# Optimization experiments

Hardware: AMD Instinct MI355X
Metric: run time of the kernel (lower is better)

The kernel has to match this reference:

```python
import jax, jax.numpy as jnp
import numpy as np

SIGMA = 5.0


def setup_inputs() -> dict:
    key = jax.random.key(0)
    ks = jax.random.split(key, 10)
    D, H, K0, K1 = 2048, 2048, 16, 8
    return {
        "inputs": jax.random.normal(ks[0], (1, D), jnp.float32),
        "cluster_center": jax.random.normal(ks[1], (K0, D), jnp.float32),
        "leaf_weight_u": jax.random.normal(ks[2], (K0, D, H), jnp.float32),
        "leaf_bias_u": jax.random.normal(ks[3], (K0, H), jnp.float32),
        "no_leaf_weight_i": jax.random.normal(ks[4], (K1, H), jnp.float32),
        "no_leaf_bias_i": jax.random.normal(ks[5], (K1,), jnp.float32),
        "no_leaf_weight_u": jax.random.normal(ks[6], (K1, H, H), jnp.float32),
        "no_leaf_bias_u": jax.random.normal(ks[7], (K1, H), jnp.float32),
        "root_weight_u": jax.random.normal(ks[8], (H, H), jnp.float32),
        "root_bias_u": jax.random.normal(ks[9], (1, H), jnp.float32),
    }


def reference(inputs, cluster_center, leaf_weight_u, leaf_bias_u,
              no_leaf_weight_i, no_leaf_bias_i, no_leaf_weight_u,
              no_leaf_bias_u, root_weight_u, root_bias_u):
    x = inputs[0]  # (D,)
    # soft assignment to cluster centers: exp(-||x-c||^2/(2*sigma)) / sum(...)
    diff = x[None, :] - cluster_center               # (K0, D)
    sq = jnp.sum(diff * diff, axis=-1)               # (K0,)
    assign = jax.nn.softmax(-sq / (2.0 * SIGMA))     # (K0,)
    # leaf cells: assignment-weighted tanh projections
    value_u = jnp.tanh(jnp.einsum('d,kdh->kh', x, leaf_weight_u) + leaf_bias_u)  # (K0, H)
    c_leaf = assign[:, None] * value_u               # (K0, H)
    # non-leaf gating: softmax over cluster_layer_1 per leaf
    gate_logits = jnp.einsum('kh,jh->kj', c_leaf, no_leaf_weight_i) + no_leaf_bias_i[None, :]  # (K0, K1)
    gate = jax.nn.softmax(gate_logits, axis=1)       # (K0, K1)
    u = jnp.tanh(jnp.einsum('kh,jhg->kjg', c_leaf, no_leaf_weight_u) + no_leaf_bias_u[None, :, :])  # (K0, K1, H)
    c_no_leaf = jnp.sum(gate[:, :, None] * u, axis=0)  # sum over K0 -> (K1, H)
    # root: sum over cluster_layer_1
    root = jnp.tanh(c_no_leaf @ root_weight_u + root_bias_u)  # (K1, H)
    root_c = jnp.sum(root, axis=0, keepdims=True)    # (1, H)
    return (root_c, root_c)
```

## Files before the change

### kernel.cpp

```cpp
#include <hip/hip_runtime.h>
#include <math.h>

#define D   2048
#define H   2048
#define K0  16
#define KJ  8

#define SKIP_THR 1e-7f

#define WS_ASSIGN 0
#define WS_GATE   64
#define WS_CLEAF  256
#define WS_PLEAF  33024
#define WS_PNL    1081600
#define WS_CNL    5275904
#define WS_PROOT  5292288
#define WS_TMP    5816576

__global__ void k_assign(const float* __restrict__ x, const float* __restrict__ cc,
                         float* __restrict__ ws) {
    int t = threadIdx.x, w = t >> 6, l = t & 63;
    const float4* c4 = (const float4*)(cc + w * D);
    const float4* x4 = (const float4*)x;
    float a = 0.f;
#pragma unroll
    for (int i = 0; i < 8; ++i) {
        float4 xv = x4[l + i * 64];
        float4 cv = c4[l + i * 64];
        float dx = xv.x - cv.x, dy = xv.y - cv.y;
        float dz = xv.z - cv.z, dw = xv.w - cv.w;
        a += dx * dx + dy * dy + dz * dz + dw * dw;
    }
#pragma unroll
    for (int off = 32; off > 0; off >>= 1) a += __shfl_down(a, off);
    __shared__ float sq[K0];
    if (l == 0) sq[w] = a;
    __syncthreads();
    if (t == 0) {
        float v[K0], m = -1e30f;
#pragma unroll
        for (int k = 0; k < K0; ++k) { v[k] = -sq[k] * 0.1f; m = fmaxf(m, v[k]); }
        float s = 0.f;
#pragma unroll
        for (int k = 0; k < K0; ++k) { v[k] = expf(v[k] - m); s += v[k]; }
        float inv = 1.0f / s;
#pragma unroll
        for (int k = 0; k < K0; ++k) ws[WS_ASSIGN + k] = v[k] * inv;
    }
}

__global__ void k_leaf_partial(const float* __restrict__ x, const float* __restrict__ W,
                               float* __restrict__ ws) {
    const int k = blockIdx.x;
    if (ws[WS_ASSIGN + k] < SKIP_THR) return;
    const int h0 = blockIdx.y * 1024;
    const int d0 = blockIdx.z * 64;
    __shared__ float xs[64];
    int t = threadIdx.x;
    if (t < 64) xs[t] = x[d0 + t];
    __syncthreads();
    int h = h0 + t * 4;
    const float* Wp = W + ((size_t)k * D + d0) * (size_t)H + h;
    float4 acc = make_float4(0.f, 0.f, 0.f, 0.f);
#pragma unroll 16
    for (int dd = 0; dd < 64; ++dd) {
        float4 w = *(const float4*)(Wp + (size_t)dd * H);
        float xv = xs[dd];
        acc.x += xv * w.x; acc.y += xv * w.y; acc.z += xv * w.z; acc.w += xv * w.w;
    }
    *(float4*)(ws + WS_PLEAF + ((size_t)(blockIdx.z * K0 + k) << 11) + h) = acc;
}

__global__ void k_cleaf(const float* __restrict__ lb, float* __restrict__ ws) {
    int idx = blockIdx.x * 256 + threadIdx.x;
    int k = idx >> 11, h = idx & (H - 1);
    float az = ws[WS_ASSIGN + k];
    float v = 0.f;
    if (az >= SKIP_THR) {
        float s = 0.f;
#pragma unroll
        for (int dc = 0; dc < 32; ++dc)
            s += ws[WS_PLEAF + ((size_t)(dc * K0 + k) << 11) + h];
        v = tanhf(s + lb[k * H + h]) * az;
    }
    ws[WS_CLEAF + k * H + h] = v;
}

__global__ void k_gate(const float* __restrict__ Wi, const float* __restrict__ bi,
                       float* __restrict__ ws) {
    int k = blockIdx.x;
    int t = threadIdx.x;
    const float* cl = ws + WS_CLEAF + k * H;
    float acc[KJ];
#pragma unroll
    for (int j = 0; j < KJ; ++j) acc[j] = 0.f;
    for (int h = t; h < H; h += 256) {
        float c = cl[h];
#pragma unroll
        for (int j = 0; j < KJ; ++j) acc[j] += c * Wi[j * H + h];
    }
    __shared__ float red[KJ][256];
#pragma unroll
    for (int j = 0; j < KJ; ++j) red[j][t] = acc[j];
    __syncthreads();
    for (int s = 128; s > 0; s >>= 1) {
        if (t < s) {
#pragma unroll
            for (int j = 0; j < KJ; ++j) red[j][t] += red[j][t + s];
        }
        __syncthreads();
    }
    if (t == 0) {
        float l[KJ], m = -1e30f;
#pragma unroll
        for (int j = 0; j < KJ; ++j) { l[j] = red[j][0] + bi[j]; m = fmaxf(m, l[j]); }
        float s = 0.f;
#pragma unroll
        for (int j = 0; j < KJ; ++j) { l[j] = expf(l[j] - m); s += l[j]; }
        float inv = 1.0f / s;
#pragma unroll
        for (int j = 0; j < KJ; ++j) ws[WS_GATE + k * KJ + j] = l[j] * inv;
    }
}

__global__ void k_nl_partial(const float* __restrict__ Wn, float* __restrict__ ws) {
    const int j  = blockIdx.x;
    const int g0 = blockIdx.y * 512;
    const int h0 = blockIdx.z * 128;
    __shared__ float cls[K0][128];
    int t = threadIdx.x;
    for (int i = t; i < K0 * 128; i += 256) {
        int k = i >> 7, hh = i & 127;
        cls[k][hh] = ws[WS_CLEAF + k * H + h0 + hh];
    }
    __syncthreads();
    int g = g0 + t * 2;
    const float* Wp = Wn + ((size_t)j * H + h0) * (size_t)H + g;
    float2 acc[K0];
#pragma unroll
    for (int k = 0; k < K0; ++k) { acc[k].x = 0.f; acc[k].y = 0.f; }
#pragma unroll 8
    for (int hh = 0; hh < 128; ++hh) {
        float2 w = *(const float2*)(Wp + (size_t)hh * H);
#pragma unroll
        for (int k = 0; k < K0; ++k) {
            float c = cls[k][hh];
            acc[k].x += c * w.x; acc[k].y += c * w.y;
        }
    }
#pragma unroll
    for (int k = 0; k < K0; ++k)
        *(float2*)(ws + WS_PNL + ((size_t)((blockIdx.z * KJ + j) * K0 + k) << 11) + g) = acc[k];
}

__global__ void k_cnl(const float* __restrict__ nb, float* __restrict__ ws) {
    int idx = blockIdx.x * 128 + threadIdx.x;
    int j = idx >> 11, g = idx & (H - 1);
    float bias = nb[j * H + g];
    float out = 0.f;
#pragma unroll
    for (int k = 0; k < K0; ++k) {
        float s = 0.f;
#pragma unroll
        for (int hc = 0; hc < 16; ++hc)
            s += ws[WS_PNL + ((size_t)((hc * KJ + j) * K0 + k) << 11) + g];
        out += ws[WS_GATE + k * KJ + j] * tanhf(s + bias);
    }
    ws[WS_CNL + j * H + g] = out;
}

__global__ void k_root_partial(const float* __restrict__ Wr, float* __restrict__ ws) {
    const int g2t = blockIdx.x;
    const int g0  = blockIdx.y * 64;
    __shared__ float cns[KJ][64];
    int t = threadIdx.x;
    for (int i = t; i < KJ * 64; i += 256) {
        int j = i >> 6, gg = i & 63;
        cns[j][gg] = ws[WS_CNL + j * H + g0 + gg];
    }
    __syncthreads();
    int g2 = g2t * 512 + t * 2;
    float2 acc[KJ];
#pragma unroll
    for (int j = 0; j < KJ; ++j) { acc[j].x = 0.f; acc[j].y = 0.f; }
#pragma unroll 8
    for (int gg = 0; gg < 64; ++gg) {
        float2 w = *(const float2*)(Wr + (size_t)(g0 + gg) * H + g2);
#pragma unroll
        for (int j = 0; j < KJ; ++j) {
            float c = cns[j][gg];
            acc[j].x += c * w.x; acc[j].y += c * w.y;
        }
    }
#pragma unroll
    for (int j = 0; j < KJ; ++j)
        *(float2*)(ws + WS_PROOT + ((size_t)(blockIdx.y * KJ + j) << 11) + g2) = acc[j];
}

__global__ void k_root_tanh(const float* __restrict__ rb, float* __restrict__ ws) {
    int j  = blockIdx.x;
    int g2 = blockIdx.y * 256 + threadIdx.x;
    float s = 0.f;
#pragma unroll
    for (int gc = 0; gc < 32; ++gc)
        s += ws[WS_PROOT + ((size_t)(gc * KJ + j) << 11) + g2];
    ws[WS_TMP + j * H + g2] = tanhf(s + rb[g2]);
}

__global__ void k_final(float* __restrict__ ws, float* __restrict__ out) {
    int g2 = blockIdx.x * 256 + threadIdx.x;
    float tot = 0.f;
#pragma unroll
    for (int j = 0; j < KJ; ++j) tot += ws[WS_TMP + j * H + g2];
    out[g2] = tot;
    out[H + g2] = tot;
}

extern "C" void kernel_launch(void* const* d_in, const int* in_sizes, int n_in,
                              void* d_out, int out_size, void* d_ws, size_t ws_size,
                              hipStream_t stream) {
    const float* x  = (const float*)d_in[0];
    const float* cc = (const float*)d_in[1];
    const float* lw = (const float*)d_in[2];
    const float* lb = (const float*)d_in[3];
    const float* wi = (const float*)d_in[4];
    const float* bi = (const float*)d_in[5];
    const float* wn = (const float*)d_in[6];
    const float* nb = (const float*)d_in[7];
    const float* wr = (const float*)d_in[8];
    const float* rb = (const float*)d_in[9];
    float* out = (float*)d_out;
    float* ws  = (float*)d_ws;

    k_assign      <<<1, 1024, 0, stream>>>(x, cc, ws);
    k_leaf_partial<<<dim3(16, 2, 32), 256, 0, stream>>>(x, lw, ws);
    k_cleaf       <<<128, 256, 0, stream>>>(lb, ws);
    k_gate        <<<16, 256, 0, stream>>>(wi, bi, ws);
    k_nl_partial  <<<dim3(8, 4, 16), 256, 0, stream>>>(wn, ws);
    k_cnl         <<<128, 128, 0, stream>>>(nb, ws);
    k_root_partial<<<dim3(4, 32), 256, 0, stream>>>(wr, ws);
    k_root_tanh   <<<dim3(8, 8), 256, 0, stream>>>(rb, ws);
    k_final       <<<8, 256, 0, stream>>>(ws, out);
}
```

Measured before the change: 500.9 us.

## Fuse all stages into one cooperative kernel with grid-wide syncs

Replaces the nine separate kernel launches with a single cooperative kernel of 512 blocks. The stages are separated by grid.sync, and the assignment softmax is recomputed in every block from the stored squared distances. The goal is to remove per-launch overhead and inter-kernel gaps. The cost is grid-sync latency, fixed work partitioning that leaves many blocks idle in the small stages, and a launch-bounds occupancy constraint. The original multi-kernel path stays as a fallback if the cooperative launch fails.

```diff
diff --git a/kernel.cpp b/kernel.cpp
--- a/kernel.cpp
+++ b/kernel.cpp
@@ -1,5 +1,8 @@
 #include <hip/hip_runtime.h>
+#include <hip/hip_cooperative_groups.h>
 #include <math.h>
+
+namespace cg = cooperative_groups;
 
 #define D   2048
 #define H   2048
@@ -8,7 +11,9 @@
 
 #define SKIP_THR 1e-7f
 
-#define WS_ASSIGN 0
+#define NBLK 512
+
+#define WS_SQ     0
 #define WS_GATE   64
 #define WS_CLEAF  256
 #define WS_PLEAF  33024
@@ -17,6 +22,212 @@
 #define WS_PROOT  5292288
 #define WS_TMP    5816576
 
+__device__ __forceinline__ void calc_assign(const float* __restrict__ ws, float a[K0]) {
+    float m = -1e30f;
+#pragma unroll
+    for (int k = 0; k < K0; ++k) { a[k] = -ws[WS_SQ + k] * 0.1f; m = fmaxf(m, a[k]); }
+    float s = 0.f;
+#pragma unroll
+    for (int k = 0; k < K0; ++k) { a[k] = expf(a[k] - m); s += a[k]; }
+    float inv = 1.0f / s;
+#pragma unroll
+    for (int k = 0; k < K0; ++k) a[k] *= inv;
+}
+
+__global__ __launch_bounds__(256, 2) void fused_kernel(
+    const float* __restrict__ x,  const float* __restrict__ cc,
+    const float* __restrict__ lw, const float* __restrict__ lb,
+    const float* __restrict__ wi, const float* __restrict__ bi,
+    const float* __restrict__ wn, const float* __restrict__ nb,
+    const float* __restrict__ wr, const float* __restrict__ rb,
+    float* __restrict__ out, float* __restrict__ ws)
+{
+    cg::grid_group grid = cg::this_grid();
+    __shared__ float smem[2048];
+    const int bid = blockIdx.x, t = threadIdx.x;
+
+    if (bid < K0) {
+        const float4* x4 = (const float4*)x;
+        const float4* c4 = (const float4*)(cc + bid * D);
+        float acc = 0.f;
+#pragma unroll
+        for (int i = 0; i < 2; ++i) {
+            float4 xv = x4[t + 256 * i], cv = c4[t + 256 * i];
+            float dx = xv.x - cv.x, dy = xv.y - cv.y;
+            float dz = xv.z - cv.z, dw = xv.w - cv.w;
+            acc += dx * dx + dy * dy + dz * dz + dw * dw;
+        }
+#pragma unroll
+        for (int off = 32; off > 0; off >>= 1) acc += __shfl_down(acc, off);
+        if ((t & 63) == 0) smem[t >> 6] = acc;
+        __syncthreads();
+        if (t == 0) ws[WS_SQ + bid] = smem[0] + smem[1] + smem[2] + smem[3];
+    }
+    grid.sync();
+
+    float a[K0];
+    calc_assign(ws, a);
+
+    for (int u = bid; u < 1024; u += NBLK) {
+        int k = u >> 6;
+        if (a[k] < SKIP_THR) continue;
+        int ht = (u >> 5) & 1, dc = u & 31;
+        int d0 = dc * 64, h0 = ht * 1024;
+        __syncthreads();
+        if (t < 64) smem[t] = x[d0 + t];
+        __syncthreads();
+        int h = h0 + t * 4;
+        const float* Wp = lw + ((size_t)k * D + d0) * (size_t)H + h;
+        float4 acc = make_float4(0.f, 0.f, 0.f, 0.f);
+#pragma unroll 16
+        for (int dd = 0; dd < 64; ++dd) {
+            float4 w4 = *(const float4*)(Wp + (size_t)dd * H);
+            float xv = smem[dd];
+            acc.x += xv * w4.x; acc.y += xv * w4.y;
+            acc.z += xv * w4.z; acc.w += xv * w4.w;
+        }
+        *(float4*)(ws + WS_PLEAF + ((size_t)(dc * K0 + k) << 11) + h) = acc;
+    }
+    grid.sync();
+
+    if (bid < K0) {
+        const int k = bid;
+        const float az = a[k];
+        float logit[KJ];
+#pragma unroll
+        for (int j = 0; j < KJ; ++j) logit[j] = 0.f;
+#pragma unroll
+        for (int i = 0; i < 8; ++i) {
+            int h = t + i * 256;
+            float v = 0.f;
+            if (az >= SKIP_THR) {
+                float s = 0.f;
+#pragma unroll
+                for (int dc = 0; dc < 32; ++dc)
+                    s += ws[WS_PLEAF + ((size_t)(dc * K0 + k) << 11) + h];
+                v = tanhf(s + lb[k * H + h]) * az;
+            }
+            ws[WS_CLEAF + k * H + h] = v;
+#pragma unroll
+            for (int j = 0; j < KJ; ++j) logit[j] += v * wi[j * H + h];
+        }
+        __syncthreads();
+#pragma unroll
+        for (int j = 0; j < KJ; ++j) smem[j * 256 + t] = logit[j];
+        __syncthreads();
+        for (int s = 128; s > 0; s >>= 1) {
+            if (t < s) {
+#pragma unroll
+                for (int j = 0; j < KJ; ++j)
+                    smem[j * 256 + t] += smem[j * 256 + t + s];
+            }
+            __syncthreads();
+        }
+        if (t == 0) {
+            float l[KJ], m = -1e30f;
+#pragma unroll
+            for (int j = 0; j < KJ; ++j) { l[j] = smem[j * 256] + bi[j]; m = fmaxf(m, l[j]); }
+            float s = 0.f;
+#pragma unroll
+            for (int j = 0; j < KJ; ++j) { l[j] = expf(l[j] - m); s += l[j]; }
+            float inv = 1.0f / s;
+#pragma unroll
+            for (int j = 0; j < KJ; ++j) ws[WS_GATE + k * KJ + j] = l[j] * inv;
+        }
+    }
+    grid.sync();
+
+    {
+        const int j  = bid >> 6;
+        const int gt = (bid >> 4) & 3;
+        const int hc = bid & 15;
+        for (int i = t; i < K0 * 128; i += 256)
+            smem[i] = ws[WS_CLEAF + (i >> 7) * H + hc * 128 + (i & 127)];
+        __syncthreads();
+        int g = gt * 512 + t * 2;
+        const float* Wp = wn + ((size_t)j * H + hc * 128) * (size_t)H + g;
+        float2 acc[K0];
+#pragma unroll
+        for (int k = 0; k < K0; ++k) { acc[k].x = 0.f; acc[k].y = 0.f; }
+#pragma unroll 8
+        for (int hh = 0; hh < 128; ++hh) {
+            float2 w2 = *(const float2*)(Wp + (size_t)hh * H);
+#pragma unroll
+            for (int k = 0; k < K0; ++k) {
+                float c = smem[k * 128 + hh];
+                acc[k].x += c * w2.x; acc[k].y += c * w2.y;
+            }
+        }
+#pragma unroll
+        for (int k = 0; k < K0; ++k)
+            *(float2*)(ws + WS_PNL + ((size_t)((hc * KJ + j) * K0 + k) << 11) + g) = acc[k];
+    }
+    grid.sync();
+
+    if (bid < 64) {
+        int idx = bid * 256 + t;
+        int j = idx >> 11, g = idx & (H - 1);
+        float bias = nb[j * H + g];
+        float o = 0.f;
+#pragma unroll
+        for (int k = 0; k < K0; ++k) {
+            float s = 0.f;
+#pragma unroll
+            for (int hc = 0; hc < 16; ++hc)
+                s += ws[WS_PNL + ((size_t)((hc * KJ + j) * K0 + k) << 11) + g];
+            o += ws[WS_GATE + k * KJ + j] * tanhf(s + bias);
+        }
+        ws[WS_CNL + j * H + g] = o;
+    }
+    grid.sync();
+
+    if (bid < 128) {
+        const int g2t = bid >> 5, gc = bid & 31;
+        for (int i = t; i < KJ * 64; i += 256)
+            smem[i] = ws[WS_CNL + (i >> 6) * H + gc * 64 + (i & 63)];
+        __syncthreads();
+        int g2 = g2t * 512 + t * 2;
+        float2 acc[KJ];
+#pragma unroll
+        for (int j = 0; j < KJ; ++j) { acc[j].x = 0.f; acc[j].y = 0.f; }
+#pragma unroll 8
+        for (int gg = 0; gg < 64; ++gg) {
+            float2 w2 = *(const float2*)(wr + (size_t)(gc * 64 + gg) * H + g2);
+#pragma unroll
+            for (int j = 0; j < KJ; ++j) {
+                float c = smem[j * 64 + gg];
+                acc[j].x += c * w2.x; acc[j].y += c * w2.y;
+            }
+        }
+#pragma unroll
+        for (int j = 0; j < KJ; ++j)
+            *(float2*)(ws + WS_PROOT + ((size_t)(gc * KJ + j) << 11) + g2) = acc[j];
+    }
+    grid.sync();
+
+    if (bid < 16) {
+        int g2 = bid * 128 + (t & 127);
+        int jh = t >> 7;
+        float part = 0.f;
+#pragma unroll
+        for (int jj = 0; jj < 4; ++jj) {
+            int j = jh * 4 + jj;
+            float s = 0.f;
+#pragma unroll
+            for (int gc = 0; gc < 32; ++gc)
+                s += ws[WS_PROOT + ((size_t)(gc * KJ + j) << 11) + g2];
+            part += tanhf(s + rb[g2]);
+        }
+        smem[t] = part;
+        __syncthreads();
+        if (t < 128) {
+            float tot = smem[t] + smem[t + 128];
+            out[g2] = tot;
+            out[H + g2] = tot;
+        }
+    }
+}
+
 __global__ void k_assign(const float* __restrict__ x, const float* __restrict__ cc,
                          float* __restrict__ ws) {
     int t = threadIdx.x, w = t >> 6, l = t & 63;
@@ -45,14 +256,14 @@
         for (int k = 0; k < K0; ++k) { v[k] = expf(v[k] - m); s += v[k]; }
         float inv = 1.0f / s;
 #pragma unroll
-        for (int k = 0; k < K0; ++k) ws[WS_ASSIGN + k] = v[k] * inv;
+        for (int k = 0; k < K0; ++k) ws[WS_SQ + k] = v[k] * inv;
     }
 }
 
 __global__ void k_leaf_partial(const float* __restrict__ x, const float* __restrict__ W,
                                float* __restrict__ ws) {
     const int k = blockIdx.x;
-    if (ws[WS_ASSIGN + k] < SKIP_THR) return;
+    if (ws[WS_SQ + k] < SKIP_THR) return;
     const int h0 = blockIdx.y * 1024;
     const int d0 = blockIdx.z * 64;
     __shared__ float xs[64];
@@ -74,7 +285,7 @@
 __global__ void k_cleaf(const float* __restrict__ lb, float* __restrict__ ws) {
     int idx = blockIdx.x * 256 + threadIdx.x;
     int k = idx >> 11, h = idx & (H - 1);
-    float az = ws[WS_ASSIGN + k];
+    float az = ws[WS_SQ + k];
     float v = 0.f;
     if (az >= SKIP_THR) {
         float s = 0.f;
@@ -230,15 +441,22 @@
     const float* wr = (const float*)d_in[8];
     const float* rb = (const float*)d_in[9];
     float* out = (float*)d_out;
-    float* ws  = (float*)d_ws;
-
-    k_assign      <<<1, 1024, 0, stream>>>(x, cc, ws);
-    k_leaf_partial<<<dim3(16, 2, 32), 256, 0, stream>>>(x, lw, ws);
-    k_cleaf       <<<128, 256, 0, stream>>>(lb, ws);
-    k_gate        <<<16, 256, 0, stream>>>(wi, bi, ws);
-    k_nl_partial  <<<dim3(8, 4, 16), 256, 0, stream>>>(wn, ws);
-    k_cnl         <<<128, 128, 0, stream>>>(nb, ws);
-    k_root_partial<<<dim3(4, 32), 256, 0, stream>>>(wr, ws);
-    k_root_tanh   <<<dim3(8, 8), 256, 0, stream>>>(rb, ws);
-    k_final       <<<8, 256, 0, stream>>>(ws, out);
-}
+    float* wsf = (float*)d_ws;
+
+    void* args[] = {(void*)&x,  (void*)&cc, (void*)&lw, (void*)&lb,
+                    (void*)&wi, (void*)&bi, (void*)&wn, (void*)&nb,
+                    (void*)&wr, (void*)&rb, (void*)&out, (void*)&wsf};
+    hipError_t e = hipLaunchCooperativeKernel((const void*)fused_kernel,
+                                              dim3(NBLK), dim3(256), args, 0, stream);
+    if (e != hipSuccess) {
+        k_assign      <<<1, 1024, 0, stream>>>(x, cc, wsf);
+        k_leaf_partial<<<dim3(16, 2, 32), 256, 0, stream>>>(x, lw, wsf);
+        k_cleaf       <<<128, 256, 0, stream>>>(lb, wsf);
+        k_gate        <<<16, 256, 0, stream>>>(wi, bi, wsf);
+        k_nl_partial  <<<dim3(8, 4, 16), 256, 0, stream>>>(wn, wsf);
+        k_cnl         <<<128, 128, 0, stream>>>(nb, wsf);
+        k_root_partial<<<dim3(4, 32), 256, 0, stream>>>(wr, wsf);
+        k_root_tanh   <<<dim3(8, 8), 256, 0, stream>>>(rb, wsf);
+        k_final       <<<8, 256, 0, stream>>>(wsf, out);
+    }
+}
```

After: 846.1 us. 1.69x slower.
